# Performance work log

Measured on AMD Instinct MI355X. Metric: run time of the kernel, lower is better.

Reference implementation:

```python
import jax, jax.numpy as jnp
import numpy as np

K = 20
HID = 64
NUM_CLASSES = 50
BIG = 1e10  # effectively-infinite distance for self-loop exclusion


def knn_idx(x, k):
    # x: [N, d] -> idx: [N, k] indices of k nearest neighbors in feature space (excluding self)
    sq = jnp.sum(x * x, axis=1)
    dist = sq[:, None] + sq[None, :] - 2.0 * (x @ x.T)  # [N, N]
    n = x.shape[0]
    dist = dist.at[jnp.arange(n), jnp.arange(n)].set(BIG)
    _, idx = jax.lax.top_k(-dist, k)
    return idx


def edge_conv(x, k, W, b):
    # DynamicEdgeConv: message = relu(Linear(cat[x_i, x_j - x_i])), aggr = max over k neighbors
    idx = knn_idx(x, k)                      # [N, k]
    xj = x[idx]                              # [N, k, d] neighbor gather
    xi = jnp.broadcast_to(x[:, None, :], xj.shape)
    feat = jnp.concatenate([xi, xj - xi], axis=-1)   # [N, k, 2d]
    h = jax.nn.relu(jnp.einsum('nkf,fo->nko', feat, W) + b)
    return jnp.max(h, axis=1)                # [N, out]


def setup_inputs() -> dict:
    key = jax.random.key(0)
    ks = jax.random.split(key, 16)
    def lin(kw, fan_in, fan_out):
        s = 1.0 / np.sqrt(fan_in)
        return jax.random.uniform(kw, (fan_in, fan_out), jnp.float32, -s, s)
    inp = {
        'x':  jax.random.normal(ks[0], (8192, 3), jnp.float32),
        'W1': lin(ks[1], 2 * 3, HID),      'b1': jnp.zeros((HID,), jnp.float32),
        'W2': lin(ks[2], 2 * HID, HID),    'b2': jnp.zeros((HID,), jnp.float32),
        'W3': lin(ks[3], 2 * HID, HID),    'b3': jnp.zeros((HID,), jnp.float32),
        'Wl': lin(ks[4], 3 * HID, 1024),   'bl': jnp.zeros((1024,), jnp.float32),
        'Wm1': lin(ks[5], 1024, 256),      'bm1': jnp.zeros((256,), jnp.float32),
        'Wm2': lin(ks[6], 256, 128),       'bm2': jnp.zeros((128,), jnp.float32),
        'Wo': lin(ks[7], 128, NUM_CLASSES),'bo': jnp.zeros((NUM_CLASSES,), jnp.float32),
    }
    return inp


def reference(x, W1, b1, W2, b2, W3, b3, Wl, bl, Wm1, bm1, Wm2, bm2, Wo, bo):
    x1 = edge_conv(x, K, W1, b1)     # [N, 64], kNN on raw 3-D points
    x2 = edge_conv(x1, K, W2, b2)    # [N, 64], kNN recomputed in feature space
    x3 = edge_conv(x2, K, W3, b3)    # [N, 64]
    h = jnp.concatenate([x1, x2, x3], axis=1)            # [N, 192]
    h = jax.nn.relu(h @ Wl + bl)                         # lin1: MLP([192, 1024])
    h = jax.nn.relu(h @ Wm1 + bm1)                       # MLP([1024, 256]) (dropout: eval mode)
    h = jax.nn.relu(h @ Wm2 + bm2)                       # MLP([256, 128])
    out = h @ Wo + bo                                    # final Linear
    return jax.nn.log_softmax(out, axis=-1)
```

## Files before the change

kernel.cpp:

```cpp
#include <hip/hip_runtime.h>
#include <math.h>

#define NPTS 8192
#define KNN 20
#define NLISTS 32

#define OFF_SQ   0
#define OFF_IDX  8192
#define OFF_A    172032
#define OFF_B    696320
#define OFF_CAT  1220608
#define OFF_H1   2793472
#define OFF_H2   11182080
#define OFF_H3   13279232
#define OFF_PART OFF_H1
#define OFF_PACK (OFF_H1 + 5242880)
#define PACK_ELEMS 262144
#define OFF_WT   OFF_A

typedef __attribute__((ext_vector_type(8))) short bf16x8;
typedef __attribute__((ext_vector_type(16))) float f32x16;

__device__ inline unsigned umed3(unsigned a, unsigned b, unsigned c) {
    unsigned d;
    asm("v_med3_u32 %0, %1, %2, %3" : "=v"(d) : "v"(a), "v"(b), "v"(c));
    return d;
}

__device__ inline unsigned short f2bf(float f) {
    unsigned u = __float_as_uint(f);
    u += 0x7FFFu + ((u >> 16) & 1u);
    return (unsigned short)(u >> 16);
}

__device__ inline void tsplit(float x, unsigned short& hi, unsigned short& lo) {
    unsigned u = __float_as_uint(x);
    hi = (unsigned short)(u >> 16);
    float d = x - __uint_as_float(u & 0xFFFF0000u);
    lo = (unsigned short)(__float_as_uint(d) >> 16);
}

__global__ __launch_bounds__(256)
void setup_kernel(const float* __restrict__ x, float* __restrict__ sq,
                  unsigned short* __restrict__ Xhi, unsigned short* __restrict__ Xlo,
                  unsigned short* __restrict__ Yhi, unsigned short* __restrict__ Ylo) {
    const int b = blockIdx.x;
    if (b < 256) {
        int t = (b * 256 + threadIdx.x) * 2;
        int n = t >> 4, k = t & 15;
        float xv[2];
        xv[0] = (k < 3) ? x[(size_t)n * 3 + k] : 0.f;
        xv[1] = (k + 1 < 3) ? x[(size_t)n * 3 + k + 1] : 0.f;
        ushort2 hx, lx, hy, ly;
        unsigned short* hxp = (unsigned short*)&hx;
        unsigned short* lxp = (unsigned short*)&lx;
        unsigned short* hyp = (unsigned short*)&hy;
        unsigned short* lyp = (unsigned short*)&ly;
        #pragma unroll
        for (int e = 0; e < 2; ++e) {
            float xx = xv[e];
            unsigned short hi = f2bf(xx);
            float hif = __uint_as_float((unsigned)hi << 16);
            unsigned short lo = f2bf(xx - hif);
            float y = -2.f * xx;
            unsigned short yhi = f2bf(y);
            float yhif = __uint_as_float((unsigned)yhi << 16);
            unsigned short ylo = f2bf(y - yhif);
            hxp[e] = hi; lxp[e] = lo; hyp[e] = yhi; lyp[e] = ylo;
        }
        *(ushort2*)&Xhi[t] = hx;
        *(ushort2*)&Xlo[t] = lx;
        *(ushort2*)&Yhi[t] = hy;
        *(ushort2*)&Ylo[t] = ly;
    } else {
        int n = (b - 256) * 256 + threadIdx.x;
        float a = x[(size_t)n * 3], bb = x[(size_t)n * 3 + 1], c = x[(size_t)n * 3 + 2];
        sq[n] = fmaf(a, a, fmaf(bb, bb, c * c));
    }
}

__global__ __launch_bounds__(256)
void wprep_kernel(const float* __restrict__ Wl, const float* __restrict__ Wm1,
                  const float* __restrict__ Wm2,
                  unsigned short* __restrict__ WlT_hi, unsigned short* __restrict__ WlT_lo,
                  unsigned short* __restrict__ Wm1T_hi, unsigned short* __restrict__ Wm1T_lo,
                  unsigned short* __restrict__ Wm2T_hi, unsigned short* __restrict__ Wm2T_lo) {
    const int b = blockIdx.x;
    const float* W; unsigned short *Thi, *Tlo; int t, K, nmask, nbits;
    if (b < 768)       { W = Wl;  Thi = WlT_hi;  Tlo = WlT_lo;  t = b * 256 + threadIdx.x;          K = 192;  nbits = 10; }
    else if (b < 1792) { W = Wm1; Thi = Wm1T_hi; Tlo = Wm1T_lo; t = (b - 768) * 256 + threadIdx.x;  K = 1024; nbits = 8; }
    else               { W = Wm2; Thi = Wm2T_hi; Tlo = Wm2T_lo; t = (b - 1792) * 256 + threadIdx.x; K = 256;  nbits = 7; }
    nmask = (1 << nbits) - 1;
    int k = t >> nbits, n = t & nmask;
    float xx = W[t];
    unsigned short hi = f2bf(xx);
    float hif = __uint_as_float((unsigned)hi << 16);
    unsigned short lo = f2bf(xx - hif);
    Thi[(size_t)n * K + k] = hi;
    Tlo[(size_t)n * K + k] = lo;
}

#define PROCESS(Cv, j0base)                                                    \
    do {                                                                       \
        _Pragma("unroll")                                                      \
        for (int q = 0; q < 4; ++q) {                                          \
            _Pragma("unroll")                                                  \
            for (int t = 0; t < 4; ++t) {                                      \
                const int j = (j0base) + h * 4 + q * 8 + t;                    \
                float dd = fmaxf((Cv)[q * 4 + t], 0.f);                        \
                unsigned key = (__float_as_uint(dd) & 0xFFFFE000u) | (unsigned)j; \
                if (j == bi) key = 0xFFFFFFFFu;                                \
                _Pragma("unroll")                                              \
                for (int p = KNN - 1; p >= 1; --p)                             \
                    top[p] = umed3(key, top[p - 1], top[p]);                   \
                top[0] = min(top[0], key);                                     \
            }                                                                  \
        }                                                                      \
    } while (0)

template<int KP>
__global__ __launch_bounds__(256, 2)
void knnA_mfma(const unsigned short* __restrict__ Yhi, const unsigned short* __restrict__ Ylo,
               const unsigned short* __restrict__ Xhi, const unsigned short* __restrict__ Xlo,
               const float* __restrict__ sq, unsigned int* __restrict__ part) {
    constexpr int NS = KP / 16;
    constexpr int NT = 8;
    const int wave = threadIdx.x >> 6, lane = threadIdx.x & 63;
    const int col = lane & 31;
    const int h   = lane >> 5;
    const int bi  = (blockIdx.x * 4 + wave) * 32 + col;
    const int jbase = blockIdx.y * 256;

    bf16x8 bhi[NS], blo[NS];
    #pragma unroll
    for (int s = 0; s < NS; ++s) {
        bhi[s] = *(const bf16x8*)&Xhi[(size_t)bi * KP + s * 16 + h * 8];
        blo[s] = *(const bf16x8*)&Xlo[(size_t)bi * KP + s * 16 + h * 8];
    }
    const float sqi = sq[bi];

    unsigned top[KNN];
    #pragma unroll
    for (int k = 0; k < KNN; ++k) top[k] = 0xFFFFFFFFu;

    bf16x8 fA[NS], fB[NS], lo[NS];
    f32x16 CCa, CCb;

    {
        const size_t a0 = (size_t)(jbase + col) * KP + h * 8;
        #pragma unroll
        for (int s = 0; s < NS; ++s)
            fA[s] = *(const bf16x8*)&Yhi[a0 + s * 16];
    }

    #pragma unroll 1
    for (int jt2 = 0; jt2 < NT; jt2 += 2) {
        const int j0 = jbase + jt2 * 32;
        const int aj = j0 + col;

        #pragma unroll
        for (int s = 0; s < NS; ++s)
            fB[s] = *(const bf16x8*)&Yhi[(size_t)(aj + 32) * KP + s * 16 + h * 8];
        #pragma unroll
        for (int s = 0; s < NS; ++s)
            lo[s] = *(const bf16x8*)&Ylo[(size_t)aj * KP + s * 16 + h * 8];
        float4 e0 = *(const float4*)&sq[j0 + h * 4];
        float4 e1 = *(const float4*)&sq[j0 + h * 4 + 8];
        float4 e2 = *(const float4*)&sq[j0 + h * 4 + 16];
        float4 e3 = *(const float4*)&sq[j0 + h * 4 + 24];

        if (jt2 > 0) PROCESS(CCb, j0 - 32);

        CCa[0] = sqi + e0.x; CCa[1] = sqi + e0.y; CCa[2]  = sqi + e0.z; CCa[3]  = sqi + e0.w;
        CCa[4] = sqi + e1.x; CCa[5] = sqi + e1.y; CCa[6]  = sqi + e1.z; CCa[7]  = sqi + e1.w;
        CCa[8] = sqi + e2.x; CCa[9] = sqi + e2.y; CCa[10] = sqi + e2.z; CCa[11] = sqi + e2.w;
        CCa[12] = sqi + e3.x; CCa[13] = sqi + e3.y; CCa[14] = sqi + e3.z; CCa[15] = sqi + e3.w;
        #pragma unroll
        for (int s = 0; s < NS; ++s) {
            CCa = __builtin_amdgcn_mfma_f32_32x32x16_bf16(fA[s], bhi[s], CCa, 0, 0, 0);
            CCa = __builtin_amdgcn_mfma_f32_32x32x16_bf16(fA[s], blo[s], CCa, 0, 0, 0);
            CCa = __builtin_amdgcn_mfma_f32_32x32x16_bf16(lo[s], bhi[s], CCa, 0, 0, 0);
        }

        if (jt2 + 2 < NT) {
            #pragma unroll
            for (int s = 0; s < NS; ++s)
                fA[s] = *(const bf16x8*)&Yhi[(size_t)(aj + 64) * KP + s * 16 + h * 8];
        }
        #pragma unroll
        for (int s = 0; s < NS; ++s)
            lo[s] = *(const bf16x8*)&Ylo[(size_t)(aj + 32) * KP + s * 16 + h * 8];
        float4 o0 = *(const float4*)&sq[j0 + 32 + h * 4];
        float4 o1 = *(const float4*)&sq[j0 + 32 + h * 4 + 8];
        float4 o2 = *(const float4*)&sq[j0 + 32 + h * 4 + 16];
        float4 o3 = *(const float4*)&sq[j0 + 32 + h * 4 + 24];

        PROCESS(CCa, j0);

        CCb[0] = sqi + o0.x; CCb[1] = sqi + o0.y; CCb[2]  = sqi + o0.z; CCb[3]  = sqi + o0.w;
        CCb[4] = sqi + o1.x; CCb[5] = sqi + o1.y; CCb[6]  = sqi + o1.z; CCb[7]  = sqi + o1.w;
        CCb[8] = sqi + o2.x; CCb[9] = sqi + o2.y; CCb[10] = sqi + o2.z; CCb[11] = sqi + o2.w;
        CCb[12] = sqi + o3.x; CCb[13] = sqi + o3.y; CCb[14] = sqi + o3.z; CCb[15] = sqi + o3.w;
        #pragma unroll
        for (int s = 0; s < NS; ++s) {
            CCb = __builtin_amdgcn_mfma_f32_32x32x16_bf16(fB[s], bhi[s], CCb, 0, 0, 0);
            CCb = __builtin_amdgcn_mfma_f32_32x32x16_bf16(fB[s], blo[s], CCb, 0, 0, 0);
            CCb = __builtin_amdgcn_mfma_f32_32x32x16_bf16(lo[s], bhi[s], CCb, 0, 0, 0);
        }
    }
    PROCESS(CCb, jbase + (NT - 1) * 32);

    {
        bool done = false;
        #pragma unroll
        for (int k = 0; k < KNN; ++k) {
            unsigned c = __shfl_xor(top[k], 32);
            if (!done) done = __all(c >= top[KNN - 1]);
            if (!done) {
                #pragma unroll
                for (int p = KNN - 1; p >= 1; --p)
                    top[p] = umed3(c, top[p - 1], top[p]);
                top[0] = min(top[0], c);
            }
        }
    }

    if (h == 0) {
        unsigned* o = part + ((size_t)bi * NLISTS + blockIdx.y) * KNN;
        #pragma unroll
        for (int k = 0; k < KNN; ++k) o[k] = top[k];
    }
}

template<int D>
__global__ __launch_bounds__(256)
void knnBfeat_kernel(const unsigned int* __restrict__ part, int* __restrict__ idx_out,
                     const float* __restrict__ X, int stride, const float* __restrict__ W,
                     float* __restrict__ A, float* __restrict__ B) {
    const int wave = threadIdx.x >> 6, lane = threadIdx.x & 63;
    if (blockIdx.x < 1024) {
        const int half = lane >> 5;
        const int l = lane & 31;
        const int row = (blockIdx.x * 4 + wave) * 2 + half;

        unsigned top[KNN];
        const unsigned* p = part + ((size_t)row * NLISTS + l) * KNN;
        #pragma unroll
        for (int k = 0; k < KNN; k += 4) {
            uint4 v = *(const uint4*)(p + k);
            top[k] = v.x; top[k + 1] = v.y; top[k + 2] = v.z; top[k + 3] = v.w;
        }

        #pragma unroll
        for (int mi = 0; mi < 5; ++mi) {
            const int m = 1 << mi;
            bool done = false;
            #pragma unroll
            for (int k = 0; k < KNN; ++k) {
                unsigned c = __shfl_xor(top[k], m);
                if (!done) done = __all(c >= top[KNN - 1]);
                if (!done) {
                    #pragma unroll
                    for (int q = KNN - 1; q >= 1; --q)
                        top[q] = umed3(c, top[q - 1], top[q]);
                    top[0] = min(top[0], c);
                }
            }
        }

        if (l == 0) {
            #pragma unroll
            for (int k = 0; k < KNN; ++k)
                idx_out[(size_t)row * KNN + k] = (int)(top[k] & 0x1FFFu);
        }
    } else {
        const int n = (blockIdx.x - 1024) * 4 + wave;
        float a = 0.f, b = 0.f;
        const float* xp = X + (size_t)n * stride;
        #pragma unroll
        for (int f = 0; f < D; ++f) {
            float xf = xp[f];
            a = fmaf(xf, W[(size_t)f * 64 + lane], a);
            b = fmaf(xf, W[(size_t)(D + f) * 64 + lane], b);
        }
        A[(size_t)n * 64 + lane] = a;
        B[(size_t)n * 64 + lane] = b;
    }
}

template<bool PACKS>
__global__ __launch_bounds__(256)
void edge_fuse_kernel(const float* __restrict__ A, const float* __restrict__ B,
                      const int* __restrict__ idx, const float* __restrict__ bias,
                      float* __restrict__ out, int colofs,
                      unsigned short* __restrict__ catHi, unsigned short* __restrict__ catLo,
                      float* __restrict__ sqo,
                      unsigned short* __restrict__ Xhi, unsigned short* __restrict__ Xlo,
                      unsigned short* __restrict__ Yhi, unsigned short* __restrict__ Ylo) {
    const int wave = threadIdx.x >> 6, lane = threadIdx.x & 63;
    const int n = blockIdx.x * 4 + wave;
    const float base = A[(size_t)n * 64 + lane] - B[(size_t)n * 64 + lane] + bias[lane];
    float m = -INFINITY;
    #pragma unroll 4
    for (int k = 0; k < KNN; ++k) {
        int j = idx[(size_t)n * KNN + k];
        m = fmaxf(m, base + B[(size_t)j * 64 + lane]);
    }
    m = fmaxf(m, 0.f);
    out[(size_t)n * 192 + colofs + lane] = m;

    unsigned short chi, clo;
    tsplit(m, chi, clo);
    catHi[(size_t)n * 192 + colofs + lane] = chi;
    catLo[(size_t)n * 192 + colofs + lane] = clo;

    if constexpr (PACKS) {
        float s = m * m;
        #pragma unroll
        for (int off = 32; off; off >>= 1) s += __shfl_xor(s, off);
        if (lane == 0) sqo[n] = s;

        unsigned short hi = f2bf(m);
        float hif = __uint_as_float((unsigned)hi << 16);
        unsigned short lo = f2bf(m - hif);
        float y = -2.f * m;
        unsigned short yhi = f2bf(y);
        float yhif = __uint_as_float((unsigned)yhi << 16);
        unsigned short ylo = f2bf(y - yhif);
        Xhi[(size_t)n * 64 + lane] = hi;
        Xlo[(size_t)n * 64 + lane] = lo;
        Yhi[(size_t)n * 64 + lane] = yhi;
        Ylo[(size_t)n * 64 + lane] = ylo;
    }
}

template<int K, int N, int CTW, bool SPLIT_OUT>
__global__ __launch_bounds__(256, 3)
void gemm_mfma(const unsigned short* __restrict__ Ahi, const unsigned short* __restrict__ Alo,
               const unsigned short* __restrict__ Whi, const unsigned short* __restrict__ Wlo,
               const float* __restrict__ bias, float* __restrict__ C,
               unsigned short* __restrict__ Chi, unsigned short* __restrict__ Clo) {
    const int wave = threadIdx.x >> 6, lane = threadIdx.x & 63;
    const int col = lane & 31, h = lane >> 5;
    const int r0 = blockIdx.x * 32;
    const int nb = blockIdx.y * (CTW * 128) + wave * (CTW * 32);
    const size_t abase = (size_t)(r0 + col) * K + h * 8;

    f32x16 acc[CTW];
    #pragma unroll
    for (int c = 0; c < CTW; ++c)
        #pragma unroll
        for (int r = 0; r < 16; ++r) acc[c][r] = 0.f;

    #pragma unroll 4
    for (int s = 0; s < K / 16; ++s) {
        bf16x8 ahi = *(const bf16x8*)&Ahi[abase + s * 16];
        bf16x8 alo = *(const bf16x8*)&Alo[abase + s * 16];
        #pragma unroll
        for (int c = 0; c < CTW; ++c) {
            const size_t wb = (size_t)(nb + c * 32 + col) * K + s * 16 + h * 8;
            bf16x8 bhi = *(const bf16x8*)&Whi[wb];
            bf16x8 blo = *(const bf16x8*)&Wlo[wb];
            acc[c] = __builtin_amdgcn_mfma_f32_32x32x16_bf16(ahi, bhi, acc[c], 0, 0, 0);
            acc[c] = __builtin_amdgcn_mfma_f32_32x32x16_bf16(alo, bhi, acc[c], 0, 0, 0);
            acc[c] = __builtin_amdgcn_mfma_f32_32x32x16_bf16(ahi, blo, acc[c], 0, 0, 0);
        }
    }

    #pragma unroll
    for (int c = 0; c < CTW; ++c) {
        const int n = nb + c * 32 + col;
        const float b = bias[n];
        #pragma unroll
        for (int q = 0; q < 4; ++q)
            #pragma unroll
            for (int t = 0; t < 4; ++t) {
                const int rl = 4 * h + 8 * q + t;
                float v = fmaxf(acc[c][q * 4 + t] + b, 0.f);
                if constexpr (SPLIT_OUT) {
                    unsigned short vh, vl;
                    tsplit(v, vh, vl);
                    Chi[(size_t)(r0 + rl) * N + n] = vh;
                    Clo[(size_t)(r0 + rl) * N + n] = vl;
                } else {
                    C[(size_t)(r0 + rl) * N + n] = v;
                }
            }
    }
}

__global__ __launch_bounds__(256)
void final_kernel(const float* __restrict__ H, const float* __restrict__ Wo,
                  const float* __restrict__ bo, float* __restrict__ out) {
    const int wave = threadIdx.x >> 6, lane = threadIdx.x & 63;
    const int n = blockIdx.x * 4 + wave;
    float v = -INFINITY;
    if (lane < 50) {
        float a = bo[lane];
        const float* h = H + (size_t)n * 128;
        #pragma unroll 4
        for (int f = 0; f < 128; ++f) a = fmaf(h[f], Wo[f * 50 + lane], a);
        v = a;
    }
    float mx = v;
    #pragma unroll
    for (int off = 32; off; off >>= 1) mx = fmaxf(mx, __shfl_xor(mx, off));
    float e = (lane < 50) ? expf(v - mx) : 0.f;
    float s = e;
    #pragma unroll
    for (int off = 32; off; off >>= 1) s += __shfl_xor(s, off);
    if (lane < 50) out[(size_t)n * 50 + lane] = v - mx - logf(s);
}

extern "C" void kernel_launch(void* const* d_in, const int* in_sizes, int n_in,
                              void* d_out, int out_size, void* d_ws, size_t ws_size,
                              hipStream_t stream) {
    const float* x   = (const float*)d_in[0];
    const float* W1  = (const float*)d_in[1];
    const float* b1  = (const float*)d_in[2];
    const float* W2  = (const float*)d_in[3];
    const float* b2  = (const float*)d_in[4];
    const float* W3  = (const float*)d_in[5];
    const float* b3  = (const float*)d_in[6];
    const float* Wl  = (const float*)d_in[7];
    const float* bl  = (const float*)d_in[8];
    const float* Wm1 = (const float*)d_in[9];
    const float* bm1 = (const float*)d_in[10];
    const float* Wm2 = (const float*)d_in[11];
    const float* bm2 = (const float*)d_in[12];
    const float* Wo  = (const float*)d_in[13];
    const float* bo  = (const float*)d_in[14];

    float* ws   = (float*)d_ws;
    float* sq   = ws + OFF_SQ;
    int*   idx  = (int*)(ws + OFF_IDX);
    float* Abuf = ws + OFF_A;
    float* Bbuf = ws + OFF_B;
    float* cat  = ws + OFF_CAT;
    unsigned int* part = (unsigned int*)(ws + OFF_PART);
    unsigned short* Phi = (unsigned short*)(ws + OFF_PACK);
    unsigned short* Plo = (unsigned short*)(ws + OFF_PACK + PACK_ELEMS);
    unsigned short* Qhi = (unsigned short*)(ws + OFF_PACK + 2 * PACK_ELEMS);
    unsigned short* Qlo = (unsigned short*)(ws + OFF_PACK + 3 * PACK_ELEMS);
    unsigned short* h1hi = (unsigned short*)(ws + OFF_H1);
    unsigned short* h1lo = (unsigned short*)(ws + OFF_H1 + 4194304);
    unsigned short* catHi = (unsigned short*)(ws + OFF_H2);
    unsigned short* catLo = (unsigned short*)(ws + OFF_H2 + 786432);
    unsigned short* h2hi = (unsigned short*)(ws + OFF_H2);
    unsigned short* h2lo = (unsigned short*)(ws + OFF_H2 + 1048576);
    float* h3   = ws + OFF_H3;
    unsigned short* WlT_hi  = (unsigned short*)(ws + OFF_WT);
    unsigned short* WlT_lo  = (unsigned short*)(ws + OFF_WT + 98304);
    unsigned short* Wm1T_hi = (unsigned short*)(ws + OFF_WT + 196608);
    unsigned short* Wm1T_lo = (unsigned short*)(ws + OFF_WT + 327680);
    unsigned short* Wm2T_hi = (unsigned short*)(ws + OFF_WT + 458752);
    unsigned short* Wm2T_lo = (unsigned short*)(ws + OFF_WT + 475136);
    float* out  = (float*)d_out;

    dim3 b256(256);
    dim3 gknn(64, 32);

    setup_kernel<<<288, b256, 0, stream>>>(x, sq, Phi, Plo, Qhi, Qlo);
    knnA_mfma<16><<<gknn, b256, 0, stream>>>(Qhi, Qlo, Phi, Plo, sq, part);
    knnBfeat_kernel<3><<<3072, b256, 0, stream>>>(part, idx, x, 3, W1, Abuf, Bbuf);
    edge_fuse_kernel<true><<<2048, b256, 0, stream>>>(Abuf, Bbuf, idx, b1, cat, 0,
                                                      catHi, catLo, sq, Phi, Plo, Qhi, Qlo);

    knnA_mfma<64><<<gknn, b256, 0, stream>>>(Qhi, Qlo, Phi, Plo, sq, part);
    knnBfeat_kernel<64><<<3072, b256, 0, stream>>>(part, idx, cat, 192, W2, Abuf, Bbuf);
    edge_fuse_kernel<true><<<2048, b256, 0, stream>>>(Abuf, Bbuf, idx, b2, cat, 64,
                                                      catHi, catLo, sq, Phi, Plo, Qhi, Qlo);

    knnA_mfma<64><<<gknn, b256, 0, stream>>>(Qhi, Qlo, Phi, Plo, sq, part);
    knnBfeat_kernel<64><<<3072, b256, 0, stream>>>(part, idx, cat + 64, 192, W3, Abuf, Bbuf);
    edge_fuse_kernel<false><<<2048, b256, 0, stream>>>(Abuf, Bbuf, idx, b3, cat, 128,
                                                       catHi, catLo, nullptr,
                                                       nullptr, nullptr, nullptr, nullptr);

    wprep_kernel<<<1920, b256, 0, stream>>>(Wl, Wm1, Wm2, WlT_hi, WlT_lo,
                                            Wm1T_hi, Wm1T_lo, Wm2T_hi, Wm2T_lo);

    dim3 g1(256, 4);
    gemm_mfma<192, 1024, 2, true><<<g1, b256, 0, stream>>>(catHi, catLo, WlT_hi, WlT_lo,
                                                           bl, nullptr, h1hi, h1lo);
    dim3 g2(256, 2);
    gemm_mfma<1024, 256, 1, true><<<g2, b256, 0, stream>>>(h1hi, h1lo, Wm1T_hi, Wm1T_lo,
                                                           bm1, nullptr, h2hi, h2lo);
    dim3 g3(256, 1);
    gemm_mfma<256, 128, 1, false><<<g3, b256, 0, stream>>>(h2hi, h2lo, Wm2T_hi, Wm2T_lo,
                                                           bm2, h3, nullptr, nullptr);
    final_kernel<<<2048, b256, 0, stream>>>(h3, Wo, bo, out);
}
```

Baseline: 472.1 us.

## Fuse kNN merge into edge kernel and feature projection into kNN kernel

Measured after the change: 522.8 us. 10.7% more time.

```diff
diff --git a/kernel.cpp b/kernel.cpp
--- a/kernel.cpp
+++ b/kernel.cpp
@@ -6,7 +6,6 @@
 #define NLISTS 32
 
 #define OFF_SQ   0
-#define OFF_IDX  8192
 #define OFF_A    172032
 #define OFF_B    696320
 #define OFF_CAT  1220608
@@ -100,7 +99,29 @@
     Tlo[(size_t)n * K + k] = lo;
 }
 
-#define PROCESS(Cv, j0base)                                                    \
+#define NET(key)                                                               \
+    do {                                                                       \
+        _Pragma("unroll")                                                      \
+        for (int p = KNN - 1; p >= 1; --p)                                     \
+            top[p] = umed3(key, top[p - 1], top[p]);                           \
+        top[0] = min(top[0], key);                                             \
+    } while (0)
+
+#define PROCESS_NX(Cv, j0base)                                                 \
+    do {                                                                       \
+        _Pragma("unroll")                                                      \
+        for (int q = 0; q < 4; ++q) {                                          \
+            _Pragma("unroll")                                                  \
+            for (int t = 0; t < 4; ++t) {                                      \
+                const int j = (j0base) + h * 4 + q * 8 + t;                    \
+                float dd = fmaxf((Cv)[q * 4 + t], 0.f);                        \
+                unsigned key = (__float_as_uint(dd) & 0xFFFFE000u) | (unsigned)j; \
+                NET(key);                                                      \
+            }                                                                  \
+        }                                                                      \
+    } while (0)
+
+#define PROCESS_EX(Cv, j0base)                                                 \
     do {                                                                       \
         _Pragma("unroll")                                                      \
         for (int q = 0; q < 4; ++q) {                                          \
@@ -110,25 +131,31 @@
                 float dd = fmaxf((Cv)[q * 4 + t], 0.f);                        \
                 unsigned key = (__float_as_uint(dd) & 0xFFFFE000u) | (unsigned)j; \
                 if (j == bi) key = 0xFFFFFFFFu;                                \
-                _Pragma("unroll")                                              \
-                for (int p = KNN - 1; p >= 1; --p)                             \
-                    top[p] = umed3(key, top[p - 1], top[p]);                   \
-                top[0] = min(top[0], key);                                     \
+                NET(key);                                                      \
             }                                                                  \
         }                                                                      \
     } while (0)
 
-template<int KP>
+#define PROCESS_SEL(Cv, j0base)                                                \
+    do {                                                                       \
+        if ((j0base) == myTile) PROCESS_EX(Cv, j0base);                        \
+        else                    PROCESS_NX(Cv, j0base);                        \
+    } while (0)
+
+template<int KP, int D>
 __global__ __launch_bounds__(256, 2)
 void knnA_mfma(const unsigned short* __restrict__ Yhi, const unsigned short* __restrict__ Ylo,
                const unsigned short* __restrict__ Xhi, const unsigned short* __restrict__ Xlo,
-               const float* __restrict__ sq, unsigned int* __restrict__ part) {
+               const float* __restrict__ sq, unsigned int* __restrict__ part,
+               const float* __restrict__ Xf, int stride, const float* __restrict__ W,
+               float* __restrict__ A, float* __restrict__ B) {
     constexpr int NS = KP / 16;
     constexpr int NT = 8;
     const int wave = threadIdx.x >> 6, lane = threadIdx.x & 63;
     const int col = lane & 31;
     const int h   = lane >> 5;
     const int bi  = (blockIdx.x * 4 + wave) * 32 + col;
+    const int myTile = bi - col;
     const int jbase = blockIdx.y * 256;
 
     bf16x8 bhi[NS], blo[NS];
@@ -169,7 +196,7 @@
         float4 e2 = *(const float4*)&sq[j0 + h * 4 + 16];
         float4 e3 = *(const float4*)&sq[j0 + h * 4 + 24];
 
-        if (jt2 > 0) PROCESS(CCb, j0 - 32);
+        if (jt2 > 0) PROCESS_SEL(CCb, j0 - 32);
 
         CCa[0] = sqi + e0.x; CCa[1] = sqi + e0.y; CCa[2]  = sqi + e0.z; CCa[3]  = sqi + e0.w;
         CCa[4] = sqi + e1.x; CCa[5] = sqi + e1.y; CCa[6]  = sqi + e1.z; CCa[7]  = sqi + e1.w;
@@ -195,7 +222,7 @@
         float4 o2 = *(const float4*)&sq[j0 + 32 + h * 4 + 16];
         float4 o3 = *(const float4*)&sq[j0 + 32 + h * 4 + 24];
 
-        PROCESS(CCa, j0);
+        PROCESS_SEL(CCa, j0);
 
         CCb[0] = sqi + o0.x; CCb[1] = sqi + o0.y; CCb[2]  = sqi + o0.z; CCb[3]  = sqi + o0.w;
         CCb[4] = sqi + o1.x; CCb[5] = sqi + o1.y; CCb[6]  = sqi + o1.z; CCb[7]  = sqi + o1.w;
@@ -208,7 +235,7 @@
             CCb = __builtin_amdgcn_mfma_f32_32x32x16_bf16(lo[s], bhi[s], CCb, 0, 0, 0);
         }
     }
-    PROCESS(CCb, jbase + (NT - 1) * 32);
+    PROCESS_SEL(CCb, jbase + (NT - 1) * 32);
 
     {
         bool done = false;
@@ -216,98 +243,79 @@
         for (int k = 0; k < KNN; ++k) {
             unsigned c = __shfl_xor(top[k], 32);
             if (!done) done = __all(c >= top[KNN - 1]);
+            if (!done) NET(c);
+        }
+    }
+
+    if (h == 0) {
+        unsigned* o = part + ((size_t)bi * NLISTS + blockIdx.y) * KNN;
+        #pragma unroll
+        for (int k = 0; k < KNN; ++k) o[k] = top[k];
+    }
+
+    {
+        const int n = blockIdx.x * 128 + blockIdx.y * 4 + wave;
+        float a = 0.f, bb = 0.f;
+        const float* xp = Xf + (size_t)n * stride;
+        #pragma unroll
+        for (int f = 0; f < D; ++f) {
+            float xf = xp[f];
+            a  = fmaf(xf, W[(size_t)f * 64 + lane], a);
+            bb = fmaf(xf, W[(size_t)(D + f) * 64 + lane], bb);
+        }
+        A[(size_t)n * 64 + lane] = a;
+        B[(size_t)n * 64 + lane] = bb;
+    }
+}
+
+template<bool PACKS>
+__global__ __launch_bounds__(256)
+void edgeB_kernel(const unsigned int* __restrict__ part,
+                  const float* __restrict__ A, const float* __restrict__ B,
+                  const float* __restrict__ bias,
+                  float* __restrict__ out, int colofs,
+                  unsigned short* __restrict__ catHi, unsigned short* __restrict__ catLo,
+                  float* __restrict__ sqo,
+                  unsigned short* __restrict__ Xhi, unsigned short* __restrict__ Xlo,
+                  unsigned short* __restrict__ Yhi, unsigned short* __restrict__ Ylo) {
+    const int wave = threadIdx.x >> 6, lane = threadIdx.x & 63;
+    const int n = blockIdx.x * 4 + wave;
+    const int l = lane & 31;
+
+    unsigned top[KNN];
+    const unsigned* p = part + ((size_t)n * NLISTS + l) * KNN;
+    #pragma unroll
+    for (int k = 0; k < KNN; k += 4) {
+        uint4 v = *(const uint4*)(p + k);
+        top[k] = v.x; top[k + 1] = v.y; top[k + 2] = v.z; top[k + 3] = v.w;
+    }
+
+    #pragma unroll
+    for (int mi = 0; mi < 5; ++mi) {
+        const int m = 1 << mi;
+        bool done = false;
+        #pragma unroll
+        for (int k = 0; k < KNN; ++k) {
+            unsigned c = __shfl_xor(top[k], m);
+            if (!done) done = __all(c >= top[KNN - 1]);
             if (!done) {
                 #pragma unroll
-                for (int p = KNN - 1; p >= 1; --p)
-                    top[p] = umed3(c, top[p - 1], top[p]);
+                for (int q = KNN - 1; q >= 1; --q)
+                    top[q] = umed3(c, top[q - 1], top[q]);
                 top[0] = min(top[0], c);
             }
         }
     }
 
-    if (h == 0) {
-        unsigned* o = part + ((size_t)bi * NLISTS + blockIdx.y) * KNN;
-        #pragma unroll
-        for (int k = 0; k < KNN; ++k) o[k] = top[k];
-    }
-}
-
-template<int D>
-__global__ __launch_bounds__(256)
-void knnBfeat_kernel(const unsigned int* __restrict__ part, int* __restrict__ idx_out,
-                     const float* __restrict__ X, int stride, const float* __restrict__ W,
-                     float* __restrict__ A, float* __restrict__ B) {
-    const int wave = threadIdx.x >> 6, lane = threadIdx.x & 63;
-    if (blockIdx.x < 1024) {
-        const int half = lane >> 5;
-        const int l = lane & 31;
-        const int row = (blockIdx.x * 4 + wave) * 2 + half;
-
-        unsigned top[KNN];
-        const unsigned* p = part + ((size_t)row * NLISTS + l) * KNN;
-        #pragma unroll
-        for (int k = 0; k < KNN; k += 4) {
-            uint4 v = *(const uint4*)(p + k);
-            top[k] = v.x; top[k + 1] = v.y; top[k + 2] = v.z; top[k + 3] = v.w;
-        }
-
-        #pragma unroll
-        for (int mi = 0; mi < 5; ++mi) {
-            const int m = 1 << mi;
-            bool done = false;
-            #pragma unroll
-            for (int k = 0; k < KNN; ++k) {
-                unsigned c = __shfl_xor(top[k], m);
-                if (!done) done = __all(c >= top[KNN - 1]);
-                if (!done) {
-                    #pragma unroll
-                    for (int q = KNN - 1; q >= 1; --q)
-                        top[q] = umed3(c, top[q - 1], top[q]);
-                    top[0] = min(top[0], c);
-                }
-            }
-        }
-
-        if (l == 0) {
-            #pragma unroll
-            for (int k = 0; k < KNN; ++k)
-                idx_out[(size_t)row * KNN + k] = (int)(top[k] & 0x1FFFu);
-        }
-    } else {
-        const int n = (blockIdx.x - 1024) * 4 + wave;
-        float a = 0.f, b = 0.f;
-        const float* xp = X + (size_t)n * stride;
-        #pragma unroll
-        for (int f = 0; f < D; ++f) {
-            float xf = xp[f];
-            a = fmaf(xf, W[(size_t)f * 64 + lane], a);
-            b = fmaf(xf, W[(size_t)(D + f) * 64 + lane], b);
-        }
-        A[(size_t)n * 64 + lane] = a;
-        B[(size_t)n * 64 + lane] = b;
-    }
-}
-
-template<bool PACKS>
-__global__ __launch_bounds__(256)
-void edge_fuse_kernel(const float* __restrict__ A, const float* __restrict__ B,
-                      const int* __restrict__ idx, const float* __restrict__ bias,
-                      float* __restrict__ out, int colofs,
-                      unsigned short* __restrict__ catHi, unsigned short* __restrict__ catLo,
-                      float* __restrict__ sqo,
-                      unsigned short* __restrict__ Xhi, unsigned short* __restrict__ Xlo,
-                      unsigned short* __restrict__ Yhi, unsigned short* __restrict__ Ylo) {
-    const int wave = threadIdx.x >> 6, lane = threadIdx.x & 63;
-    const int n = blockIdx.x * 4 + wave;
     const float base = A[(size_t)n * 64 + lane] - B[(size_t)n * 64 + lane] + bias[lane];
     float m = -INFINITY;
     #pragma unroll 4
     for (int k = 0; k < KNN; ++k) {
-        int j = idx[(size_t)n * KNN + k];
+        int j = __shfl((int)(top[k] & 0x1FFFu), 0);
         m = fmaxf(m, base + B[(size_t)j * 64 + lane]);
     }
     m = fmaxf(m, 0.f);
-    out[(size_t)n * 192 + colofs + lane] = m;
+    if (PACKS) out[(size_t)n * 192 + colofs + lane] = m;
 
     unsigned short chi, clo;
     tsplit(m, chi, clo);
@@ -433,7 +441,6 @@
 
     float* ws   = (float*)d_ws;
     float* sq   = ws + OFF_SQ;
-    int*   idx  = (int*)(ws + OFF_IDX);
     float* Abuf = ws + OFF_A;
     float* Bbuf = ws + OFF_B;
     float* cat  = ws + OFF_CAT;
@@ -461,21 +468,21 @@
     dim3 gknn(64, 32);
 
     setup_kernel<<<288, b256, 0, stream>>>(x, sq, Phi, Plo, Qhi, Qlo);
-    knnA_mfma<16><<<gknn, b256, 0, stream>>>(Qhi, Qlo, Phi, Plo, sq, part);
-    knnBfeat_kernel<3><<<3072, b256, 0, stream>>>(part, idx, x, 3, W1, Abuf, Bbuf);
-    edge_fuse_kernel<true><<<2048, b256, 0, stream>>>(Abuf, Bbuf, idx, b1, cat, 0,
-                                                      catHi, catLo, sq, Phi, Plo, Qhi, Qlo);
-
-    knnA_mfma<64><<<gknn, b256, 0, stream>>>(Qhi, Qlo, Phi, Plo, sq, part);
-    knnBfeat_kernel<64><<<3072, b256, 0, stream>>>(part, idx, cat, 192, W2, Abuf, Bbuf);
-    edge_fuse_kernel<true><<<2048, b256, 0, stream>>>(Abuf, Bbuf, idx, b2, cat, 64,
-                                                      catHi, catLo, sq, Phi, Plo, Qhi, Qlo);
-
-    knnA_mfma<64><<<gknn, b256, 0, stream>>>(Qhi, Qlo, Phi, Plo, sq, part);
-    knnBfeat_kernel<64><<<3072, b256, 0, stream>>>(part, idx, cat + 64, 192, W3, Abuf, Bbuf);
-    edge_fuse_kernel<false><<<2048, b256, 0, stream>>>(Abuf, Bbuf, idx, b3, cat, 128,
-                                                       catHi, catLo, nullptr,
-                                                       nullptr, nullptr, nullptr, nullptr);
+    knnA_mfma<16, 3><<<gknn, b256, 0, stream>>>(Qhi, Qlo, Phi, Plo, sq, part,
+                                                x, 3, W1, Abuf, Bbuf);
+    edgeB_kernel<true><<<2048, b256, 0, stream>>>(part, Abuf, Bbuf, b1, cat, 0,
+                                                  catHi, catLo, sq, Phi, Plo, Qhi, Qlo);
+
+    knnA_mfma<64, 64><<<gknn, b256, 0, stream>>>(Qhi, Qlo, Phi, Plo, sq, part,
+                                                 cat, 192, W2, Abuf, Bbuf);
+    edgeB_kernel<true><<<2048, b256, 0, stream>>>(part, Abuf, Bbuf, b2, cat, 64,
+                                                  catHi, catLo, sq, Phi, Plo, Qhi, Qlo);
+
+    knnA_mfma<64, 64><<<gknn, b256, 0, stream>>>(Qhi, Qlo, Phi, Plo, sq, part,
+                                                 cat + 64, 192, W3, Abuf, Bbuf);
+    edgeB_kernel<false><<<2048, b256, 0, stream>>>(part, Abuf, Bbuf, b3, cat, 128,
+                                                   catHi, catLo, nullptr,
+                                                   nullptr, nullptr, nullptr, nullptr);
 
     wprep_kernel<<<1920, b256, 0, stream>>>(Wl, Wm1, Wm2, WlT_hi, WlT_lo,
                                             Wm1T_hi, Wm1T_lo, Wm2T_hi, Wm2T_lo);
```
